# Optimization experiments

Measured on AMD Instinct MI355X. Metric: run time of the kernel, lower is better.

## Reference

```python
import jax, jax.numpy as jnp
import numpy as np
import math

B, S, H = 2, 2048, 2048
NH, NKV, HD = 16, 8, 128          # heads, kv heads, head_dim
GROUPS = NH // NKV                 # 2
FF = 5632
EPS = 1e-6
SCALE = 0.02


def setup_inputs() -> dict:
    key = jax.random.key(0)
    ks = jax.random.split(key, 12)
    def w(k, shape):
        return jax.random.normal(k, shape, dtype=jnp.float32) * SCALE
    # additive causal mask: 0 on/below diagonal, -inf above
    causal = jnp.where(jnp.tril(jnp.ones((S, S), dtype=bool)), 0.0, -jnp.inf)
    attention_mask = causal[None, None].astype(jnp.float32)  # [1,1,S,S]
    return {
        "hidden_states": jax.random.normal(ks[0], (B, S, H), dtype=jnp.float32),
        "attention_mask": attention_mask,
        "q_w": w(ks[1], (NH * HD, H)),      # nn.Linear convention [out, in]
        "k_w": w(ks[2], (NKV * HD, H)),
        "v_w": w(ks[3], (NKV * HD, H)),
        "o_w": w(ks[4], (H, NH * HD)),
        "gate_w": w(ks[5], (FF, H)),
        "up_w": w(ks[6], (FF, H)),
        "down_w": w(ks[7], (H, FF)),
        "ln1_w": jnp.ones((H,), dtype=jnp.float32),
        "ln2_w": jnp.ones((H,), dtype=jnp.float32),
    }


def rmsnorm(x, w):
    var = jnp.mean(jnp.square(x), axis=-1, keepdims=True)
    return x * jax.lax.rsqrt(var + EPS) * w


def attention(x, mask, q_w, k_w, v_w, o_w):
    b, s, _ = x.shape
    q = (x @ q_w.T).reshape(b, s, NH, HD).transpose(0, 2, 1, 3)    # [b,nh,s,hd]
    k = (x @ k_w.T).reshape(b, s, NKV, HD).transpose(0, 2, 1, 3)   # [b,nkv,s,hd]
    v = (x @ v_w.T).reshape(b, s, NKV, HD).transpose(0, 2, 1, 3)
    # GQA: repeat_interleave kv heads to match query heads
    k = jnp.repeat(k, GROUPS, axis=1)
    v = jnp.repeat(v, GROUPS, axis=1)
    scores = jnp.einsum("bhqd,bhkd->bhqk", q, k) / math.sqrt(HD) + mask
    probs = jax.nn.softmax(scores.astype(jnp.float32), axis=-1).astype(q.dtype)
    out = jnp.einsum("bhqk,bhkd->bhqd", probs, v)
    out = out.transpose(0, 2, 1, 3).reshape(b, s, NH * HD)
    return out @ o_w.T


def mlp(x, gate_w, up_w, down_w):
    return (jax.nn.silu(x @ gate_w.T) * (x @ up_w.T)) @ down_w.T


def reference(hidden_states, attention_mask, q_w, k_w, v_w, o_w,
              gate_w, up_w, down_w, ln1_w, ln2_w):
    # pre-norm transformer layer with residuals
    h = hidden_states + attention(rmsnorm(hidden_states, ln1_w), attention_mask,
                                  q_w, k_w, v_w, o_w)
    out = h + mlp(rmsnorm(h, ln2_w), gate_w, up_w, down_w)
    return out
```

## Files before the change

kernel.cpp:

```cpp
#include <hip/hip_runtime.h>
#include <stdint.h>

typedef __bf16 bf16_t;
typedef __bf16 bf16x8 __attribute__((ext_vector_type(8)));
typedef __bf16 bf16x4 __attribute__((ext_vector_type(4)));
typedef float  f32x4  __attribute__((ext_vector_type(4)));

#define MFMA16(a, b, c) __builtin_amdgcn_mfma_f32_16x16x32_bf16((a), (b), (c), 0, 0, 0)

__device__ __forceinline__ void load_lds16(const bf16_t* g, bf16_t* l)
{
    __builtin_amdgcn_global_load_lds(
        (const __attribute__((address_space(1))) uint32_t*)(uintptr_t)g,
        (__attribute__((address_space(3))) uint32_t*)(uint32_t)(uintptr_t)l,
        16, 0, 0);
}

__device__ __forceinline__ void lds_stage2(const bf16_t* __restrict__ Gsrc,
                                           bf16_t* Ldst, int u0,
                                           int tid, int K, int k0)
{
#pragma unroll
    for (int l = 0; l < 2; ++l) {
        int u = u0 + l * 512 + tid;
// ... 49 lines not shown
}

__global__ __launch_bounds__(256)
void rmsnorm_bf16(const bf16_t* __restrict__ X, const float* __restrict__ Wt,
                  bf16_t* __restrict__ Y)
{
    __shared__ float red[4];
    const int tid = threadIdx.x;
    const size_t row = blockIdx.x;

    bf16x8 xv = *(const bf16x8*)(X + row * 2048 + tid * 8);
    float xf[8];
    float ss = 0.f;
#pragma unroll
    for (int e = 0; e < 8; ++e) { xf[e] = (float)xv[e]; ss += xf[e] * xf[e]; }
#pragma unroll
    for (int off = 32; off; off >>= 1) ss += __shfl_xor(ss, off, 64);
    if ((tid & 63) == 0) red[tid >> 6] = ss;
    __syncthreads();
    float tot = red[0] + red[1] + red[2] + red[3];
    float scale = rsqrtf(tot * (1.f / 2048.f) + 1e-6f);

    f32x4 w0 = *(const f32x4*)(Wt + tid * 8);
    f32x4 w1 = *(const f32x4*)(Wt + tid * 8 + 4);
    bf16x8 yv;
#pragma unroll
    for (int e = 0; e < 4; ++e) {
        yv[e]     = (bf16_t)(xf[e] * scale * w0[e]);
        yv[e + 4] = (bf16_t)(xf[e + 4] * scale * w1[e]);
    }
    *(bf16x8*)(Y + row * 2048 + tid * 8) = yv;
}

__global__ __launch_bounds__(256, 2)
void gemm_bb(const bf16_t* __restrict__ A, const bf16_t* __restrict__ W,
             const float* __restrict__ Rf, const bf16_t* __restrict__ Rb,
             bf16_t* __restrict__ Cb, float* __restrict__ Cf,
             int M, int N, int K, int mode)
{
    __shared__ bf16_t As[128 * 64];
    __shared__ bf16_t Ws[128 * 64];

    const int tid  = threadIdx.x;
    const int lane = tid & 63, wave = tid >> 6;
    const int quad = lane >> 4, l16 = lane & 15;
    const int m0 = blockIdx.y * 128, n0 = blockIdx.x * 128;
    const int wm = (wave >> 1) * 64, wn = (wave & 1) * 64;

    const bf16_t* Ab = A + (size_t)(m0 + (tid >> 3)) * K + ((tid & 7) << 3);
    const bf16_t* Wb = W + (size_t)(n0 + (tid >> 3)) * K + ((tid & 7) << 3);

    f32x4 acc[4][4] = {};

    for (int k0 = 0; k0 < K; k0 += 64) {
        __syncthreads();
#pragma unroll
        for (int i = 0; i < 4; ++i) {
            load_lds16(Ab + (size_t)(i * 32) * K + k0, As + (i * 256 + tid) * 8);
            load_lds16(Wb + (size_t)(i * 32) * K + k0, Ws + (i * 256 + tid) * 8);
        }
        __syncthreads();

#pragma unroll
        for (int ks = 0; ks < 64; ks += 32) {
            bf16x8 af[4], bfr[4];
#pragma unroll
            for (int i = 0; i < 4; ++i)
                af[i] = *(const bf16x8*)(As + (wm + i * 16 + l16) * 64 + ks + quad * 8);
#pragma unroll
            for (int j = 0; j < 4; ++j)
                bfr[j] = *(const bf16x8*)(Ws + (wn + j * 16 + l16) * 64 + ks + quad * 8);
#pragma unroll
            for (int i = 0; i < 4; ++i)
#pragma unroll
                for (int j = 0; j < 4; ++j)
                    acc[i][j] = MFMA16(af[i], bfr[j], acc[i][j]);
        }
    }

#pragma unroll
    for (int i = 0; i < 4; ++i)
#pragma unroll
        for (int j = 0; j < 4; ++j)
#pragma unroll
            for (int r = 0; r < 4; ++r) {
                size_t row = (size_t)(m0 + wm + i * 16 + quad * 4 + r);
                size_t col = (size_t)(n0 + wn + j * 16 + l16);
                float v = acc[i][j][r];
                if (mode == 1) v += Rf[row * (size_t)N + col];
                if (mode == 2)
                    Cf[row * (size_t)N + col] = v + (float)Rb[row * (size_t)N + col];
                else
                    Cb[row * (size_t)N + col] = (bf16_t)v;
            }
}

__global__ __launch_bounds__(512, 2)
void gemm8(const bf16_t* __restrict__ A, const bf16_t* __restrict__ W,
           const float* __restrict__ Rf, const bf16_t* __restrict__ Rb,
           bf16_t* __restrict__ Cb, float* __restrict__ Cf,
           int M, int N, int K, int mode)
{
    __shared__ bf16_t As[2][256 * 64];
    __shared__ bf16_t Ws[2][128 * 64];

    const int tid  = threadIdx.x;
    const int lane = tid & 63, wave = tid >> 6;
    const int quad = lane >> 4, l16 = lane & 15;
    const int wr = wave >> 1, wc = wave & 1;

    const int lid = (int)blockIdx.x;
    const int swz = (lid & 7) * 32 + (lid >> 3);
    const int bym = swz >> 4;
    const int bxn = swz & 15;
    const int m0 = bym * 256, n0 = bxn * 128;

    const bf16_t* Ab = A + (size_t)m0 * K;
    const bf16_t* Wb = W + (size_t)n0 * K;

    const int xsw  = (l16 & 7) << 3;
    const int aoff = (wr * 64 + l16) * 64;
    const int boff = (wc * 64 + l16) * 64;

    f32x4 acc[4][4] = {};

    lds_stage2(Ab, As[0], 0,    tid, K, 0);
    lds_stage2(Ab, As[0], 1024, tid, K, 0);
    lds_stage2(Wb, Ws[0], 0,    tid, K, 0);

    const int NT = K >> 6;
    for (int t = 0; t < NT; ++t) {
        const int b  = t & 1;
        const int kn = (t + 1) << 6;
        const bool pf = (t + 1 < NT);
        bf16_t* An = As[1 - b];
        bf16_t* Wn = Ws[1 - b];

        if (pf) {
            lds_stage2(Ab, An, 0, tid, K, kn);
            asm volatile("s_waitcnt vmcnt(2)" ::: "memory");
        } else {
            asm volatile("s_waitcnt vmcnt(0)" ::: "memory");
        }
        __builtin_amdgcn_s_barrier();

        const bf16_t* Asb = As[b];
        const bf16_t* Wsb = Ws[b];

#pragma unroll
        for (int ks = 0; ks < 2; ++ks) {
            const int kxo = (ks * 32 + quad * 8) ^ xsw;
            bf16x8 af[4], bf_[4];
#pragma unroll
            for (int i = 0; i < 4; ++i)
                af[i] = *(const bf16x8*)(Asb + aoff + i * 1024 + kxo);
#pragma unroll
            for (int j = 0; j < 4; ++j)
                bf_[j] = *(const bf16x8*)(Wsb + boff + j * 1024 + kxo);
            if (pf) {
                if (ks == 0) lds_stage2(Ab, An, 1024, tid, K, kn);
                else         lds_stage2(Wb, Wn, 0,    tid, K, kn);
            }
            __builtin_amdgcn_s_barrier();
            __builtin_amdgcn_s_setprio(1);
#pragma unroll
            for (int i = 0; i < 4; ++i)
#pragma unroll
                for (int j = 0; j < 4; ++j)
                    acc[i][j] = MFMA16(af[i], bf_[j], acc[i][j]);
            __builtin_amdgcn_s_setprio(0);
            __builtin_amdgcn_s_barrier();
        }
    }

#pragma unroll
    for (int i = 0; i < 4; ++i)
#pragma unroll
        for (int j = 0; j < 4; ++j)
#pragma unroll
            for (int r = 0; r < 4; ++r) {
                size_t row = (size_t)(m0 + wr * 64 + i * 16 + quad * 4 + r);
                size_t col = (size_t)(n0 + wc * 64 + j * 16 + l16);
                float v = acc[i][j][r];
                if (mode == 1) v += Rf[row * (size_t)N + col];
                if (mode == 2)
                    Cf[row * (size_t)N + col] = v + (float)Rb[row * (size_t)N + col];
                else
                    Cb[row * (size_t)N + col] = (bf16_t)v;
            }
}

__global__ __launch_bounds__(512, 2)
void gateup8(const bf16_t* __restrict__ A, const bf16_t* __restrict__ G,
             const bf16_t* __restrict__ U, bf16_t* __restrict__ C,
             int M, int N, int K)
{
    __shared__ bf16_t As[2][256 * 64];
    __shared__ bf16_t Gs[2][128 * 64];
    __shared__ bf16_t Us[2][128 * 64];

    const int tid  = threadIdx.x;
    const int lane = tid & 63;
    const int wave = tid >> 6;
    const int quad = lane >> 4, l16 = lane & 15;
    const int wr = wave >> 2, wc = wave & 3;

    const int lid = (int)blockIdx.x;
    const int nwg = (M >> 8) * (N >> 7);
    const int cpx = nwg >> 3;
    const int swz = (lid & 7) * cpx + (lid >> 3);
    const int bxn = swz >> 4;
    const int bym = swz & 15;
    const int m0 = bym * 256, n0 = bxn * 128;

    const bf16_t* Ab = A + (size_t)m0 * K;
    const bf16_t* Gb = G + (size_t)n0 * K;
    const bf16_t* Ub = U + (size_t)n0 * K;

    const int xsw  = (l16 & 7) << 3;
    const int aoff = (wr * 128 + l16) * 64;
    const int boff = (wc * 32 + l16) * 64;

    f32x4 accg[8][2] = {};
    f32x4 accu[8][2] = {};

    lds_stage2(Ab, As[0], 0,    tid, K, 0);
    lds_stage2(Ab, As[0], 1024, tid, K, 0);
    lds_stage2(Gb, Gs[0], 0,    tid, K, 0);
    lds_stage2(Ub, Us[0], 0,    tid, K, 0);

    const int NT = K >> 6;
    for (int t = 0; t < NT; ++t) {
        const int b  = t & 1;
        const int kn = (t + 1) << 6;
        const bool pf = (t + 1 < NT);
        bf16_t* An = As[1 - b];
        bf16_t* Gn = Gs[1 - b];
        bf16_t* Un = Us[1 - b];

        if (pf) {
            lds_stage2(Ab, An, 0, tid, K, kn);
            asm volatile("s_waitcnt vmcnt(2)" ::: "memory");
        } else {
            asm volatile("s_waitcnt vmcnt(0)" ::: "memory");
        }
        __builtin_amdgcn_s_barrier();

        const bf16_t* Asb = As[b];
        const bf16_t* Gsb = Gs[b];
        const bf16_t* Usb = Us[b];

        bf16x8 af[4], bg[2], bu[2];

        {
            const int kxo = (quad * 8) ^ xsw;
#pragma unroll
            for (int i = 0; i < 4; ++i)
                af[i] = *(const bf16x8*)(Asb + aoff + i * 1024 + kxo);
#pragma unroll
            for (int j = 0; j < 2; ++j) {
                bg[j] = *(const bf16x8*)(Gsb + boff + j * 1024 + kxo);
                bu[j] = *(const bf16x8*)(Usb + boff + j * 1024 + kxo);
            }
        }
        if (pf) lds_stage2(Ab, An, 1024, tid, K, kn);
        __builtin_amdgcn_s_barrier();
        __builtin_amdgcn_s_setprio(1);
#pragma unroll
        for (int i = 0; i < 4; ++i)
#pragma unroll
            for (int j = 0; j < 2; ++j) {
                accg[i][j] = MFMA16(af[i], bg[j], accg[i][j]);
                accu[i][j] = MFMA16(af[i], bu[j], accu[i][j]);
            }
        __builtin_amdgcn_s_setprio(0);
        __builtin_amdgcn_s_barrier();

        {
            const int kxo = (quad * 8) ^ xsw;
#pragma unroll
            for (int i = 0; i < 4; ++i)
                af[i] = *(const bf16x8*)(Asb + aoff + (i + 4) * 1024 + kxo);
        }
        if (pf) lds_stage2(Gb, Gn, 0, tid, K, kn);
        __builtin_amdgcn_s_barrier();
        __builtin_amdgcn_s_setprio(1);
#pragma unroll
        for (int i = 0; i < 4; ++i)
#pragma unroll
            for (int j = 0; j < 2; ++j) {
                accg[i + 4][j] = MFMA16(af[i], bg[j], accg[i + 4][j]);
                accu[i + 4][j] = MFMA16(af[i], bu[j], accu[i + 4][j]);
            }
        __builtin_amdgcn_s_setprio(0);
        __builtin_amdgcn_s_barrier();

        {
            const int kxo = (32 + quad * 8) ^ xsw;
#pragma unroll
            for (int i = 0; i < 4; ++i)
                af[i] = *(const bf16x8*)(Asb + aoff + i * 1024 + kxo);
#pragma unroll
            for (int j = 0; j < 2; ++j) {
                bg[j] = *(const bf16x8*)(Gsb + boff + j * 1024 + kxo);
                bu[j] = *(const bf16x8*)(Usb + boff + j * 1024 + kxo);
            }
        }
        if (pf) lds_stage2(Ub, Un, 0, tid, K, kn);
        __builtin_amdgcn_s_barrier();
        __builtin_amdgcn_s_setprio(1);
#pragma unroll
        for (int i = 0; i < 4; ++i)
#pragma unroll
            for (int j = 0; j < 2; ++j) {
                accg[i][j] = MFMA16(af[i], bg[j], accg[i][j]);
                accu[i][j] = MFMA16(af[i], bu[j], accu[i][j]);
            }
        __builtin_amdgcn_s_setprio(0);
        __builtin_amdgcn_s_barrier();

        {
            const int kxo = (32 + quad * 8) ^ xsw;
#pragma unroll
            for (int i = 0; i < 4; ++i)
                af[i] = *(const bf16x8*)(Asb + aoff + (i + 4) * 1024 + kxo);
        }
        __builtin_amdgcn_s_barrier();
        __builtin_amdgcn_s_setprio(1);
#pragma unroll
        for (int i = 0; i < 4; ++i)
#pragma unroll
            for (int j = 0; j < 2; ++j) {
                accg[i + 4][j] = MFMA16(af[i], bg[j], accg[i + 4][j]);
                accu[i + 4][j] = MFMA16(af[i], bu[j], accu[i + 4][j]);
            }
        __builtin_amdgcn_s_setprio(0);
        __builtin_amdgcn_s_barrier();
    }

#pragma unroll
    for (int i = 0; i < 8; ++i)
#pragma unroll
        for (int j = 0; j < 2; ++j)
#pragma unroll
            for (int r = 0; r < 4; ++r) {
                size_t row = (size_t)(m0 + wr * 128 + i * 16 + quad * 4 + r);
                size_t col = (size_t)(n0 + wc * 32 + j * 16 + l16);
                float g = accg[i][j][r];
                float u = accu[i][j][r];
                float sig = 1.f / (1.f + __expf(fminf(-g, 80.f)));
                C[row * (size_t)N + col] = (bf16_t)(g * sig * u);
            }
}

__global__ __launch_bounds__(256, 2)
void gemm_bt(const bf16_t* __restrict__ A, const float* __restrict__ W,
             const float* __restrict__ Rf, const bf16_t* __restrict__ Rb,
             bf16_t* __restrict__ Cb, float* __restrict__ Cf,
             int M, int N, int K, int mode)
{
    __shared__ bf16_t As[128 * 64];
    __shared__ bf16_t Ws[128 * 64];

    const int tid  = threadIdx.x;
    const int lane = tid & 63, wave = tid >> 6;
    const int quad = lane >> 4, l16 = lane & 15;
    const int m0 = blockIdx.y * 128, n0 = blockIdx.x * 128;
    const int wm = (wave >> 1) * 64, wn = (wave & 1) * 64;

    f32x4 acc[4][4] = {};

    for (int k0 = 0; k0 < K; k0 += 64) {
        bf16x8 ra[4];
        bf16x4 rw[8];
#pragma unroll
        for (int i = 0; i < 4; ++i) {
            int u = i * 256 + tid;
            int r = u >> 3, c = (u & 7) << 3;
            ra[i] = *(const bf16x8*)(A + (size_t)(m0 + r) * K + k0 + c);
        }
#pragma unroll
        for (int i = 0; i < 8; ++i) {
            int u = i * 256 + tid;
            int r = u >> 4, c = (u & 15) << 2;
            f32x4 w4 = *(const f32x4*)(W + (size_t)(n0 + r) * K + k0 + c);
#pragma unroll
            for (int e = 0; e < 4; ++e) rw[i][e] = (bf16_t)w4[e];
        }
        __syncthreads();
#pragma unroll
        for (int i = 0; i < 4; ++i)
            *(bf16x8*)(As + (i * 256 + tid) * 8) = ra[i];
#pragma unroll
        for (int i = 0; i < 8; ++i)
            *(bf16x4*)(Ws + (i * 256 + tid) * 4) = rw[i];
        __syncthreads();

#pragma unroll
        for (int ks = 0; ks < 64; ks += 32) {
            bf16x8 af[4], bfr[4];
#pragma unroll
            for (int i = 0; i < 4; ++i)
                af[i] = *(const bf16x8*)(As + (wm + i * 16 + l16) * 64 + ks + quad * 8);
#pragma unroll
            for (int j = 0; j < 4; ++j)
                bfr[j] = *(const bf16x8*)(Ws + (wn + j * 16 + l16) * 64 + ks + quad * 8);
#pragma unroll
            for (int i = 0; i < 4; ++i)
#pragma unroll
                for (int j = 0; j < 4; ++j)
                    acc[i][j] = MFMA16(af[i], bfr[j], acc[i][j]);
        }
    }

#pragma unroll
    for (int i = 0; i < 4; ++i)
#pragma unroll
        for (int j = 0; j < 4; ++j)
#pragma unroll
            for (int r = 0; r < 4; ++r) {
                size_t row = (size_t)(m0 + wm + i * 16 + quad * 4 + r);
                size_t col = (size_t)(n0 + wn + j * 16 + l16);
                float v = acc[i][j][r];
                if (mode == 1) v += Rf[row * (size_t)N + col];
                if (mode == 2)
                    Cf[row * (size_t)N + col] = v + (float)Rb[row * (size_t)N + col];
                else
                    Cb[row * (size_t)N + col] = (bf16_t)v;
            }
}

__global__ __launch_bounds__(256, 2)
void gemm_gateup(const bf16_t* __restrict__ A, const float* __restrict__ G,
                 const float* __restrict__ U, bf16_t* __restrict__ C,
                 int M, int N, int K)
{
    __shared__ bf16_t As[128 * 64];
    __shared__ bf16_t Gs[128 * 64];
    __shared__ bf16_t Us[128 * 64];

    const int tid  = threadIdx.x;
    const int lane = tid & 63, wave = tid >> 6;
    const int quad = lane >> 4, l16 = lane & 15;
    const int m0 = blockIdx.y * 128, n0 = blockIdx.x * 128;
    const int wm = (wave >> 1) * 64, wn = (wave & 1) * 64;

    f32x4 accg[4][4] = {};
    f32x4 accu[4][4] = {};

    for (int k0 = 0; k0 < K; k0 += 64) {
        bf16x8 ra[4];
        bf16x4 rg[8], ru[8];
#pragma unroll
        for (int i = 0; i < 4; ++i) {
            int u = i * 256 + tid;
            int r = u >> 3, c = (u & 7) << 3;
            ra[i] = *(const bf16x8*)(A + (size_t)(m0 + r) * K + k0 + c);
        }
#pragma unroll
        for (int i = 0; i < 8; ++i) {
            int u = i * 256 + tid;
            int r = u >> 4, c = (u & 15) << 2;
            f32x4 g4 = *(const f32x4*)(G + (size_t)(n0 + r) * K + k0 + c);
            f32x4 u4 = *(const f32x4*)(U + (size_t)(n0 + r) * K + k0 + c);
// ... 19 lines not shown
                af[i] = *(const bf16x8*)(As + (wm + i * 16 + l16) * 64 + ks + quad * 8);
#pragma unroll
            for (int j = 0; j < 4; ++j) {
                bg[j] = *(const bf16x8*)(Gs + (wn + j * 16 + l16) * 64 + ks + quad * 8);
                bu[j] = *(const bf16x8*)(Us + (wn + j * 16 + l16) * 64 + ks + quad * 8);
            }
#pragma unroll
            for (int i = 0; i < 4; ++i)
#pragma unroll
                for (int j = 0; j < 4; ++j) {
                    accg[i][j] = MFMA16(af[i], bg[j], accg[i][j]);
                    accu[i][j] = MFMA16(af[i], bu[j], accu[i][j]);
                }
        }
    }

#pragma unroll
    for (int i = 0; i < 4; ++i)
#pragma unroll
        for (int j = 0; j < 4; ++j)
#pragma unroll
            for (int r = 0; r < 4; ++r) {
                size_t row = (size_t)(m0 + wm + i * 16 + quad * 4 + r);
                size_t col = (size_t)(n0 + wn + j * 16 + l16);
                float g = accg[i][j][r];
                float u = accu[i][j][r];
                float sig = 1.f / (1.f + __expf(fminf(-g, 80.f)));
                C[row * (size_t)N + col] = (bf16_t)(g * sig * u);
            }
}

__global__ __launch_bounds__(256, 2)
void attn_fwd(const bf16_t* __restrict__ Q, const bf16_t* __restrict__ Kg,
              const bf16_t* __restrict__ Vg, bf16_t* __restrict__ O)
{
    __shared__ bf16_t Ks[64 * 128];
    __shared__ bf16_t Vt[128 * 64];
    __shared__ bf16_t Pl[4][16 * 72];

    const int tid  = threadIdx.x;
    const int lane = tid & 63, wave = tid >> 6;
    const int quad = lane >> 4, l16 = lane & 15;
    const int bh = blockIdx.y, b = bh >> 4, h = bh & 15;

    const bf16_t* Qh = Q  + (size_t)b * 2048 * 2048 + (size_t)h * 128;
    const bf16_t* Kh = Kg + (size_t)b * 2048 * 1024 + (size_t)(h >> 1) * 128;
    const bf16_t* Vh = Vg + (size_t)b * 2048 * 1024 + (size_t)(h >> 1) * 128;

    const float scale = 0.08838834764831845f;

#pragma unroll 1
    for (int pass = 0; pass < 2; ++pass) {
        const int qt = pass ? (31 - (int)blockIdx.x) : (int)blockIdx.x;
        const int q0 = qt * 64;

        bf16x8 aq[4];
#pragma unroll
        for (int ks = 0; ks < 4; ++ks)
            aq[ks] = *(const bf16x8*)(Qh + (size_t)(q0 + wave * 16 + l16) * 2048 + ks * 32 + quad * 8);

        float m_r[4] = { -30000.f, -30000.f, -30000.f, -30000.f };
        float l_r[4] = { 0.f, 0.f, 0.f, 0.f };
        f32x4 acc_o[8] = {};

        const int ntiles = qt + 1;

        for (int t = 0; t < ntiles; ++t) {
            const int kv0 = t * 64;
            __syncthreads();
#pragma unroll
            for (int i = 0; i < 4; ++i) {
                int u = i * 256 + tid;
                int rk = u >> 4, c = (u & 15) << 3;
                *(bf16x8*)(Ks + u * 8) =
                    *(const bf16x8*)(Kh + (size_t)(kv0 + rk) * 1024 + c);
            }
#pragma unroll
            for (int it = 0; it < 4; ++it) {
                int v = it * 256 + tid;
                int d = v & 127, kb = v >> 7;
                bf16x8 vt8;
#pragma unroll
                for (int j = 0; j < 8; ++j)
                    vt8[j] = Vh[(size_t)(kv0 + kb * 8 + j) * 1024 + d];
                *(bf16x8*)(Vt + d * 64 + ((kb ^ (d & 7)) << 3)) = vt8;
            }
            __syncthreads();

            f32x4 accs[4] = {};
#pragma unroll
            for (int ks = 0; ks < 4; ++ks)
#pragma unroll
                for (int j = 0; j < 4; ++j) {
                    bf16x8 bk = *(const bf16x8*)(Ks + (j * 16 + l16) * 128 + ks * 32 + quad * 8);
                    accs[j] = MFMA16(aq[ks], bk, accs[j]);
                }

#pragma unroll
            for (int r = 0; r < 4; ++r) {
                const int qrow = q0 + wave * 16 + quad * 4 + r;
                float s[4];
                float mx = -30000.f;
#pragma unroll
                for (int j = 0; j < 4; ++j) {
                    s[j] = accs[j][r] * scale;
                    if (kv0 + j * 16 + l16 > qrow) s[j] = -30000.f;
                    mx = fmaxf(mx, s[j]);
                }
                mx = fmaxf(mx, __shfl_xor(mx, 1, 64));
                mx = fmaxf(mx, __shfl_xor(mx, 2, 64));
                mx = fmaxf(mx, __shfl_xor(mx, 4, 64));
                mx = fmaxf(mx, __shfl_xor(mx, 8, 64));
                float mnew  = fmaxf(m_r[r], mx);
                float alpha = __expf(fmaxf(m_r[r] - mnew, -80.f));
                float rs = 0.f;
#pragma unroll
                for (int j = 0; j < 4; ++j) {
                    float p = __expf(fmaxf(s[j] - mnew, -80.f));
                    rs += p;
                    Pl[wave][(quad * 4 + r) * 72 + j * 16 + l16] = (bf16_t)p;
                }
                rs += __shfl_xor(rs, 1, 64);
                rs += __shfl_xor(rs, 2, 64);
                rs += __shfl_xor(rs, 4, 64);
                rs += __shfl_xor(rs, 8, 64);
                l_r[r] = l_r[r] * alpha + rs;
                m_r[r] = mnew;
#pragma unroll
                for (int nt = 0; nt < 8; ++nt) acc_o[nt][r] *= alpha;
            }

            __syncthreads();

#pragma unroll
            for (int ks2 = 0; ks2 < 2; ++ks2) {
                bf16x8 ap = *(const bf16x8*)(&Pl[wave][l16 * 72 + ks2 * 32 + quad * 8]);
                const int kb_r = ks2 * 4 + quad;
#pragma unroll
                for (int nt = 0; nt < 8; ++nt) {
                    const int d = nt * 16 + l16;
                    bf16x8 bv = *(const bf16x8*)(Vt + d * 64 + ((kb_r ^ (d & 7)) << 3));
                    acc_o[nt] = MFMA16(ap, bv, acc_o[nt]);
                }
            }
        }

#pragma unroll
        for (int r = 0; r < 4; ++r) {
            float inv = 1.f / fmaxf(l_r[r], 1e-30f);
            size_t orow = (size_t)b * 2048 + q0 + wave * 16 + quad * 4 + r;
#pragma unroll
            for (int nt = 0; nt < 8; ++nt)
                O[orow * 2048 + h * 128 + nt * 16 + l16] = (bf16_t)(acc_o[nt][r] * inv);
        }
    }
}

extern "C" void kernel_launch(void* const* d_in, const int* in_sizes, int n_in,
                              void* d_out, int out_size, void* d_ws, size_t ws_size,
                              hipStream_t stream)
{
    const float* x   = (const float*)d_in[0];
    const float* qw  = (const float*)d_in[2];
    const float* kw  = (const float*)d_in[3];
    const float* vw  = (const float*)d_in[4];
    const float* ow  = (const float*)d_in[5];
    const float* gw  = (const float*)d_in[6];
    const float* uw  = (const float*)d_in[7];
    const float* dw  = (const float*)d_in[8];
    const float* ln1 = (const float*)d_in[9];
    const float* ln2 = (const float*)d_in[10];
    float*  out = (float*)d_out;
    bf16_t* ws  = (bf16_t*)d_ws;

    dim3 blk(256);
    const size_t NEED = 87031808ull * 2;

    if (ws_size >= NEED) {
        bf16_t* wq = ws;
        bf16_t* wk = ws + 4194304;
        bf16_t* wv = ws + 6291456;
        bf16_t* wo = ws + 8388608;
        bf16_t* wg = ws + 12582912;
        bf16_t* wu = ws + 24117248;
        bf16_t* wd = ws + 35651584;
        bf16_t* h1 = ws + 47185920;
        bf16_t* qb = ws + 55574528;
        bf16_t* kb = ws + 63963136;
        bf16_t* vb = ws + 68157440;
        bf16_t* ab = (bf16_t*)d_out;
        bf16_t* hb = qb;
        bf16_t* gb = kb;

        wconv<<<2048, blk, 0, stream>>>(qw, wq, 4194304);
        wconv<<<1024, blk, 0, stream>>>(kw, wk, 2097152);
        wconv<<<1024, blk, 0, stream>>>(vw, wv, 2097152);
        wconv<<<2048, blk, 0, stream>>>(ow, wo, 4194304);
        wconv<<<5632, blk, 0, stream>>>(gw, wg, 11534336);
        wconv<<<5632, blk, 0, stream>>>(uw, wu, 11534336);
        wconv<<<5632, blk, 0, stream>>>(dw, wd, 11534336);

        rmsnorm_f32<<<4096, blk, 0, stream>>>(x, ln1, h1);
        gemm8<<<256, dim3(512), 0, stream>>>(h1, wq, nullptr, nullptr, qb, nullptr, 4096, 2048, 2048, 0);
        gemm_bb<<<dim3( 8, 32), blk, 0, stream>>>(h1, wk, nullptr, nullptr, kb, nullptr, 4096, 1024, 2048, 0);
        gemm_bb<<<dim3( 8, 32), blk, 0, stream>>>(h1, wv, nullptr, nullptr, vb, nullptr, 4096, 1024, 2048, 0);
        attn_fwd<<<dim3(16, 32), blk, 0, stream>>>(qb, kb, vb, ab);
        gemm8<<<256, dim3(512), 0, stream>>>(ab, wo, x, nullptr, hb, nullptr, 4096, 2048, 2048, 1);
        rmsnorm_bf16<<<4096, blk, 0, stream>>>(hb, ln2, h1);
        gateup8<<<704, dim3(512), 0, stream>>>(h1, wg, wu, gb, 4096, 5632, 2048);
        gemm8<<<256, dim3(512), 0, stream>>>(gb, wd, nullptr, hb, nullptr, out, 4096, 2048, 5632, 2);
    } else {
        const size_t ME = 1ull << 20;
        bf16_t* h1 = ws;
        bf16_t* qb = ws + 8  * ME;
        bf16_t* kb = ws + 16 * ME;
        bf16_t* vb = ws + 20 * ME;
        bf16_t* ab = (bf16_t*)d_out;
        bf16_t* hb = ws + 8  * ME;
        bf16_t* gb = ws + 16 * ME;

        rmsnorm_f32<<<4096, blk, 0, stream>>>(x, ln1, h1);
        gemm_bt<<<dim3(16, 32), blk, 0, stream>>>(h1, qw, nullptr, nullptr, qb, nullptr, 4096, 2048, 2048, 0);
        gemm_bt<<<dim3( 8, 32), blk, 0, stream>>>(h1, kw, nullptr, nullptr, kb, nullptr, 4096, 1024, 2048, 0);
        gemm_bt<<<dim3( 8, 32), blk, 0, stream>>>(h1, vw, nullptr, nullptr, vb, nullptr, 4096, 1024, 2048, 0);
        attn_fwd<<<dim3(16, 32), blk, 0, stream>>>(qb, kb, vb, ab);
        gemm_bt<<<dim3(16, 32), blk, 0, stream>>>(ab, ow, x, nullptr, hb, nullptr, 4096, 2048, 2048, 1);
        rmsnorm_bf16<<<4096, blk, 0, stream>>>(hb, ln2, h1);
        gemm_gateup<<<dim3(44, 32), blk, 0, stream>>>(h1, gw, uw, gb, 4096, 5632, 2048);
        gemm_bt<<<dim3(16, 32), blk, 0, stream>>>(gb, dw, nullptr, hb, nullptr, out, 4096, 2048, 5632, 2);
    }
}
```

Measured before the change: 887.2 us.

## Fuse K/V projections into one gemm8 launch and double-buffer attention KV tiles

The separate K and V projection GEMMs (the older 128x128 gemm_bb kernel) become a single launch of the pipelined 256x128 gemm8 kernel. A new epilogue mode splits the output columns between the K and V buffers, which relies on wk and wv sitting next to each other in the workspace. The attention kernel now double-buffers its K and V^T LDS tiles with a register prefetch of the next tile, K is stored with an XOR swizzle, and one barrier per iteration is removed. gemm8's block swizzle is also generalised through an nbx parameter. The risks are higher LDS use in attention, which may lower occupancy, and a dependence on the weight layout.

```diff
diff --git a/kernel.cpp b/kernel.cpp
--- a/kernel.cpp
+++ b/kernel.cpp
@@ -105,8 +105,273 @@
     *(bf16x8*)(Y + row * 2048 + tid * 8) = yv;
 }
 
+__global__ __launch_bounds__(512, 2)
+void gemm8(const bf16_t* __restrict__ A, const bf16_t* __restrict__ W,
+           const float* __restrict__ Rf, const bf16_t* __restrict__ Rb,
+           bf16_t* __restrict__ Cb, bf16_t* __restrict__ Cb2,
+           float* __restrict__ Cf,
+           int M, int N, int K, int nbx, int mode)
+{
+    __shared__ bf16_t As[2][256 * 64];
+    __shared__ bf16_t Ws[2][128 * 64];
+
+    const int tid  = threadIdx.x;
+    const int lane = tid & 63, wave = tid >> 6;
+    const int quad = lane >> 4, l16 = lane & 15;
+    const int wr = wave >> 1, wc = wave & 1;
+
+    const int lid = (int)blockIdx.x;
+    const int nwg = (M >> 8) * nbx;
+    const int q   = nwg >> 3;
+    const int swz = (lid & 7) * q + (lid >> 3);
+    const int bxn = swz >> 4;
+    const int bym = swz & 15;
+    const int m0 = bym * 256, n0 = bxn * 128;
+
+    const bf16_t* Ab = A + (size_t)m0 * K;
+    const bf16_t* Wb = W + (size_t)n0 * K;
+
+    const int xsw  = (l16 & 7) << 3;
+    const int aoff = (wr * 64 + l16) * 64;
+    const int boff = (wc * 64 + l16) * 64;
+
+    f32x4 acc[4][4] = {};
+
+    lds_stage2(Ab, As[0], 0,    tid, K, 0);
+    lds_stage2(Ab, As[0], 1024, tid, K, 0);
+    lds_stage2(Wb, Ws[0], 0,    tid, K, 0);
+
+    const int NT = K >> 6;
+    for (int t = 0; t < NT; ++t) {
+        const int b  = t & 1;
+        const int kn = (t + 1) << 6;
+        const bool pf = (t + 1 < NT);
+        bf16_t* An = As[1 - b];
+        bf16_t* Wn = Ws[1 - b];
+
+        if (pf) {
+            lds_stage2(Ab, An, 0, tid, K, kn);
+            asm volatile("s_waitcnt vmcnt(2)" ::: "memory");
+        } else {
+            asm volatile("s_waitcnt vmcnt(0)" ::: "memory");
+        }
+        __builtin_amdgcn_s_barrier();
+
+        const bf16_t* Asb = As[b];
+        const bf16_t* Wsb = Ws[b];
+
+#pragma unroll
+        for (int ks = 0; ks < 2; ++ks) {
+            const int kxo = (ks * 32 + quad * 8) ^ xsw;
+            bf16x8 af[4], bf_[4];
+#pragma unroll
+            for (int i = 0; i < 4; ++i)
+                af[i] = *(const bf16x8*)(Asb + aoff + i * 1024 + kxo);
+#pragma unroll
+            for (int j = 0; j < 4; ++j)
+                bf_[j] = *(const bf16x8*)(Wsb + boff + j * 1024 + kxo);
+            if (pf) {
+                if (ks == 0) lds_stage2(Ab, An, 1024, tid, K, kn);
+                else         lds_stage2(Wb, Wn, 0,    tid, K, kn);
+            }
+            __builtin_amdgcn_s_barrier();
+            __builtin_amdgcn_s_setprio(1);
+#pragma unroll
+            for (int i = 0; i < 4; ++i)
+#pragma unroll
+                for (int j = 0; j < 4; ++j)
+                    acc[i][j] = MFMA16(af[i], bf_[j], acc[i][j]);
+            __builtin_amdgcn_s_setprio(0);
+            __builtin_amdgcn_s_barrier();
+        }
+    }
+
+    bf16_t* dst5 = (n0 < 1024) ? Cb : Cb2;
+
+#pragma unroll
+    for (int i = 0; i < 4; ++i)
+#pragma unroll
+        for (int j = 0; j < 4; ++j)
+#pragma unroll
+            for (int r = 0; r < 4; ++r) {
+                size_t row = (size_t)(m0 + wr * 64 + i * 16 + quad * 4 + r);
+                size_t col = (size_t)(n0 + wc * 64 + j * 16 + l16);
+                float v = acc[i][j][r];
+                if (mode == 1) v += Rf[row * (size_t)N + col];
+                if (mode == 2)
+                    Cf[row * (size_t)N + col] = v + (float)Rb[row * (size_t)N + col];
+                else if (mode == 5)
+                    dst5[row * 1024 + (col & 1023)] = (bf16_t)v;
+                else
+                    Cb[row * (size_t)N + col] = (bf16_t)v;
+            }
+}
+
+__global__ __launch_bounds__(512, 2)
+void gateup8(const bf16_t* __restrict__ A, const bf16_t* __restrict__ G,
+             const bf16_t* __restrict__ U, bf16_t* __restrict__ C,
+             int M, int N, int K)
+{
+    __shared__ bf16_t As[2][256 * 64];
+    __shared__ bf16_t Gs[2][128 * 64];
+    __shared__ bf16_t Us[2][128 * 64];
+
+    const int tid  = threadIdx.x;
+    const int lane = tid & 63;
+    const int wave = tid >> 6;
+    const int quad = lane >> 4, l16 = lane & 15;
+    const int wr = wave >> 2, wc = wave & 3;
+
+    const int lid = (int)blockIdx.x;
+    const int nwg = (M >> 8) * (N >> 7);
+    const int cpx = nwg >> 3;
+    const int swz = (lid & 7) * cpx + (lid >> 3);
+    const int bxn = swz >> 4;
+    const int bym = swz & 15;
+    const int m0 = bym * 256, n0 = bxn * 128;
+
+    const bf16_t* Ab = A + (size_t)m0 * K;
+    const bf16_t* Gb = G + (size_t)n0 * K;
+    const bf16_t* Ub = U + (size_t)n0 * K;
+
+    const int xsw  = (l16 & 7) << 3;
+    const int aoff = (wr * 128 + l16) * 64;
+    const int boff = (wc * 32 + l16) * 64;
+
+    f32x4 accg[8][2] = {};
+    f32x4 accu[8][2] = {};
+
+    lds_stage2(Ab, As[0], 0,    tid, K, 0);
+    lds_stage2(Ab, As[0], 1024, tid, K, 0);
+    lds_stage2(Gb, Gs[0], 0,    tid, K, 0);
+    lds_stage2(Ub, Us[0], 0,    tid, K, 0);
+
+    const int NT = K >> 6;
+    for (int t = 0; t < NT; ++t) {
+        const int b  = t & 1;
+        const int kn = (t + 1) << 6;
+        const bool pf = (t + 1 < NT);
+        bf16_t* An = As[1 - b];
+        bf16_t* Gn = Gs[1 - b];
+        bf16_t* Un = Us[1 - b];
+
+        if (pf) {
+            lds_stage2(Ab, An, 0, tid, K, kn);
+            asm volatile("s_waitcnt vmcnt(2)" ::: "memory");
+        } else {
+            asm volatile("s_waitcnt vmcnt(0)" ::: "memory");
+        }
+        __builtin_amdgcn_s_barrier();
+
+        const bf16_t* Asb = As[b];
+        const bf16_t* Gsb = Gs[b];
+        const bf16_t* Usb = Us[b];
+
+        bf16x8 af[4], bg[2], bu[2];
+
+        {
+            const int kxo = (quad * 8) ^ xsw;
+#pragma unroll
+            for (int i = 0; i < 4; ++i)
+                af[i] = *(const bf16x8*)(Asb + aoff + i * 1024 + kxo);
+#pragma unroll
+            for (int j = 0; j < 2; ++j) {
+                bg[j] = *(const bf16x8*)(Gsb + boff + j * 1024 + kxo);
+                bu[j] = *(const bf16x8*)(Usb + boff + j * 1024 + kxo);
+            }
+        }
+        if (pf) lds_stage2(Ab, An, 1024, tid, K, kn);
+        __builtin_amdgcn_s_barrier();
+        __builtin_amdgcn_s_setprio(1);
+#pragma unroll
+        for (int i = 0; i < 4; ++i)
+#pragma unroll
+            for (int j = 0; j < 2; ++j) {
+                accg[i][j] = MFMA16(af[i], bg[j], accg[i][j]);
+                accu[i][j] = MFMA16(af[i], bu[j], accu[i][j]);
+            }
+        __builtin_amdgcn_s_setprio(0);
+        __builtin_amdgcn_s_barrier();
+
+        {
+            const int kxo = (quad * 8) ^ xsw;
+#pragma unroll
+            for (int i = 0; i < 4; ++i)
+                af[i] = *(const bf16x8*)(Asb + aoff + (i + 4) * 1024 + kxo);
+        }
+        if (pf) lds_stage2(Gb, Gn, 0, tid, K, kn);
+        __builtin_amdgcn_s_barrier();
+        __builtin_amdgcn_s_setprio(1);
+#pragma unroll
+        for (int i = 0; i < 4; ++i)
+#pragma unroll
+            for (int j = 0; j < 2; ++j) {
+                accg[i + 4][j] = MFMA16(af[i], bg[j], accg[i + 4][j]);
+                accu[i + 4][j] = MFMA16(af[i], bu[j], accu[i + 4][j]);
+            }
+        __builtin_amdgcn_s_setprio(0);
+        __builtin_amdgcn_s_barrier();
+
+        {
+            const int kxo = (32 + quad * 8) ^ xsw;
+#pragma unroll
+            for (int i = 0; i < 4; ++i)
+                af[i] = *(const bf16x8*)(Asb + aoff + i * 1024 + kxo);
+#pragma unroll
+            for (int j = 0; j < 2; ++j) {
+                bg[j] = *(const bf16x8*)(Gsb + boff + j * 1024 + kxo);
+                bu[j] = *(const bf16x8*)(Usb + boff + j * 1024 + kxo);
+            }
+        }
+        if (pf) lds_stage2(Ub, Un, 0, tid, K, kn);
+        __builtin_amdgcn_s_barrier();
+        __builtin_amdgcn_s_setprio(1);
+#pragma unroll
+        for (int i = 0; i < 4; ++i)
+#pragma unroll
+            for (int j = 0; j < 2; ++j) {
+                accg[i][j] = MFMA16(af[i], bg[j], accg[i][j]);
+                accu[i][j] = MFMA16(af[i], bu[j], accu[i][j]);
+            }
+        __builtin_amdgcn_s_setprio(0);
+        __builtin_amdgcn_s_barrier();
+
+        {
+            const int kxo = (32 + quad * 8) ^ xsw;
+#pragma unroll
+            for (int i = 0; i < 4; ++i)
+                af[i] = *(const bf16x8*)(Asb + aoff + (i + 4) * 1024 + kxo);
+        }
+        __builtin_amdgcn_s_barrier();
+        __builtin_amdgcn_s_setprio(1);
+#pragma unroll
+        for (int i = 0; i < 4; ++i)
+#pragma unroll
+            for (int j = 0; j < 2; ++j) {
+                accg[i + 4][j] = MFMA16(af[i], bg[j], accg[i + 4][j]);
+                accu[i + 4][j] = MFMA16(af[i], bu[j], accu[i + 4][j]);
+            }
+        __builtin_amdgcn_s_setprio(0);
+        __builtin_amdgcn_s_barrier();
+    }
+
+#pragma unroll
+    for (int i = 0; i < 8; ++i)
+#pragma unroll
+        for (int j = 0; j < 2; ++j)
+#pragma unroll
+            for (int r = 0; r < 4; ++r) {
+                size_t row = (size_t)(m0 + wr * 128 + i * 16 + quad * 4 + r);
+                size_t col = (size_t)(n0 + wc * 32 + j * 16 + l16);
+                float g = accg[i][j][r];
+                float u = accu[i][j][r];
+                float sig = 1.f / (1.f + __expf(fminf(-g, 80.f)));
+                C[row * (size_t)N + col] = (bf16_t)(g * sig * u);
+            }
+}
+
 __global__ __launch_bounds__(256, 2)
-void gemm_bb(const bf16_t* __restrict__ A, const bf16_t* __restrict__ W,
+void gemm_bt(const bf16_t* __restrict__ A, const float* __restrict__ W,
              const float* __restrict__ Rf, const bf16_t* __restrict__ Rb,
              bf16_t* __restrict__ Cb, float* __restrict__ Cf,
              int M, int N, int K, int mode)
@@ -120,18 +385,32 @@
     const int m0 = blockIdx.y * 128, n0 = blockIdx.x * 128;
     const int wm = (wave >> 1) * 64, wn = (wave & 1) * 64;
 
-    const bf16_t* Ab = A + (size_t)(m0 + (tid >> 3)) * K + ((tid & 7) << 3);
-    const bf16_t* Wb = W + (size_t)(n0 + (tid >> 3)) * K + ((tid & 7) << 3);
-
     f32x4 acc[4][4] = {};
 
     for (int k0 = 0; k0 < K; k0 += 64) {
+        bf16x8 ra[4];
+        bf16x4 rw[8];
+#pragma unroll
+        for (int i = 0; i < 4; ++i) {
+            int u = i * 256 + tid;
+            int r = u >> 3, c = (u & 7) << 3;
+            ra[i] = *(const bf16x8*)(A + (size_t)(m0 + r) * K + k0 + c);
+        }
+#pragma unroll
+        for (int i = 0; i < 8; ++i) {
+            int u = i * 256 + tid;
+            int r = u >> 4, c = (u & 15) << 2;
+            f32x4 w4 = *(const f32x4*)(W + (size_t)(n0 + r) * K + k0 + c);
+#pragma unroll
+            for (int e = 0; e < 4; ++e) rw[i][e] = (bf16_t)w4[e];
+        }
         __syncthreads();
 #pragma unroll
-        for (int i = 0; i < 4; ++i) {
-            load_lds16(Ab + (size_t)(i * 32) * K + k0, As + (i * 256 + tid) * 8);
-            load_lds16(Wb + (size_t)(i * 32) * K + k0, Ws + (i * 256 + tid) * 8);
-        }
+        for (int i = 0; i < 4; ++i)
+            *(bf16x8*)(As + (i * 256 + tid) * 8) = ra[i];
+#pragma unroll
+        for (int i = 0; i < 8; ++i)
+            *(bf16x4*)(Ws + (i * 256 + tid) * 4) = rw[i];
         __syncthreads();
 
 #pragma unroll
@@ -168,341 +447,6 @@
             }
 }
 
-__global__ __launch_bounds__(512, 2)
-void gemm8(const bf16_t* __restrict__ A, const bf16_t* __restrict__ W,
-           const float* __restrict__ Rf, const bf16_t* __restrict__ Rb,
-           bf16_t* __restrict__ Cb, float* __restrict__ Cf,
-           int M, int N, int K, int mode)
-{
-    __shared__ bf16_t As[2][256 * 64];
-    __shared__ bf16_t Ws[2][128 * 64];
-
-    const int tid  = threadIdx.x;
-    const int lane = tid & 63, wave = tid >> 6;
-    const int quad = lane >> 4, l16 = lane & 15;
-    const int wr = wave >> 1, wc = wave & 1;
-
-    const int lid = (int)blockIdx.x;
-    const int swz = (lid & 7) * 32 + (lid >> 3);
-    const int bym = swz >> 4;
-    const int bxn = swz & 15;
-    const int m0 = bym * 256, n0 = bxn * 128;
-
-    const bf16_t* Ab = A + (size_t)m0 * K;
-    const bf16_t* Wb = W + (size_t)n0 * K;
-
-    const int xsw  = (l16 & 7) << 3;
-    const int aoff = (wr * 64 + l16) * 64;
-    const int boff = (wc * 64 + l16) * 64;
-
-    f32x4 acc[4][4] = {};
-
-    lds_stage2(Ab, As[0], 0,    tid, K, 0);
-    lds_stage2(Ab, As[0], 1024, tid, K, 0);
-    lds_stage2(Wb, Ws[0], 0,    tid, K, 0);
-
-    const int NT = K >> 6;
-    for (int t = 0; t < NT; ++t) {
-        const int b  = t & 1;
-        const int kn = (t + 1) << 6;
-        const bool pf = (t + 1 < NT);
-        bf16_t* An = As[1 - b];
-        bf16_t* Wn = Ws[1 - b];
-
-        if (pf) {
-            lds_stage2(Ab, An, 0, tid, K, kn);
-            asm volatile("s_waitcnt vmcnt(2)" ::: "memory");
-        } else {
-            asm volatile("s_waitcnt vmcnt(0)" ::: "memory");
-        }
-        __builtin_amdgcn_s_barrier();
-
-        const bf16_t* Asb = As[b];
-        const bf16_t* Wsb = Ws[b];
-
-#pragma unroll
-        for (int ks = 0; ks < 2; ++ks) {
-            const int kxo = (ks * 32 + quad * 8) ^ xsw;
-            bf16x8 af[4], bf_[4];
-#pragma unroll
-            for (int i = 0; i < 4; ++i)
-                af[i] = *(const bf16x8*)(Asb + aoff + i * 1024 + kxo);
-#pragma unroll
-            for (int j = 0; j < 4; ++j)
-                bf_[j] = *(const bf16x8*)(Wsb + boff + j * 1024 + kxo);
-            if (pf) {
-                if (ks == 0) lds_stage2(Ab, An, 1024, tid, K, kn);
-                else         lds_stage2(Wb, Wn, 0,    tid, K, kn);
-            }
-            __builtin_amdgcn_s_barrier();
-            __builtin_amdgcn_s_setprio(1);
-#pragma unroll
-            for (int i = 0; i < 4; ++i)
-#pragma unroll
-                for (int j = 0; j < 4; ++j)
-                    acc[i][j] = MFMA16(af[i], bf_[j], acc[i][j]);
-            __builtin_amdgcn_s_setprio(0);
-            __builtin_amdgcn_s_barrier();
-        }
-    }
-
-#pragma unroll
-    for (int i = 0; i < 4; ++i)
-#pragma unroll
-        for (int j = 0; j < 4; ++j)
-#pragma unroll
-            for (int r = 0; r < 4; ++r) {
-                size_t row = (size_t)(m0 + wr * 64 + i * 16 + quad * 4 + r);
-                size_t col = (size_t)(n0 + wc * 64 + j * 16 + l16);
-                float v = acc[i][j][r];
-                if (mode == 1) v += Rf[row * (size_t)N + col];
-                if (mode == 2)
-                    Cf[row * (size_t)N + col] = v + (float)Rb[row * (size_t)N + col];
-                else
-                    Cb[row * (size_t)N + col] = (bf16_t)v;
-            }
-}
-
-__global__ __launch_bounds__(512, 2)
-void gateup8(const bf16_t* __restrict__ A, const bf16_t* __restrict__ G,
-             const bf16_t* __restrict__ U, bf16_t* __restrict__ C,
-             int M, int N, int K)
-{
-    __shared__ bf16_t As[2][256 * 64];
-    __shared__ bf16_t Gs[2][128 * 64];
-    __shared__ bf16_t Us[2][128 * 64];
-
-    const int tid  = threadIdx.x;
-    const int lane = tid & 63;
-    const int wave = tid >> 6;
-    const int quad = lane >> 4, l16 = lane & 15;
-    const int wr = wave >> 2, wc = wave & 3;
-
-    const int lid = (int)blockIdx.x;
-    const int nwg = (M >> 8) * (N >> 7);
-    const int cpx = nwg >> 3;
-    const int swz = (lid & 7) * cpx + (lid >> 3);
-    const int bxn = swz >> 4;
-    const int bym = swz & 15;
-    const int m0 = bym * 256, n0 = bxn * 128;
-
-    const bf16_t* Ab = A + (size_t)m0 * K;
-    const bf16_t* Gb = G + (size_t)n0 * K;
-    const bf16_t* Ub = U + (size_t)n0 * K;
-
-    const int xsw  = (l16 & 7) << 3;
-    const int aoff = (wr * 128 + l16) * 64;
-    const int boff = (wc * 32 + l16) * 64;
-
-    f32x4 accg[8][2] = {};
-    f32x4 accu[8][2] = {};
-
-    lds_stage2(Ab, As[0], 0,    tid, K, 0);
-    lds_stage2(Ab, As[0], 1024, tid, K, 0);
-    lds_stage2(Gb, Gs[0], 0,    tid, K, 0);
-    lds_stage2(Ub, Us[0], 0,    tid, K, 0);
-
-    const int NT = K >> 6;
-    for (int t = 0; t < NT; ++t) {
-        const int b  = t & 1;
-        const int kn = (t + 1) << 6;
-        const bool pf = (t + 1 < NT);
-        bf16_t* An = As[1 - b];
-        bf16_t* Gn = Gs[1 - b];
-        bf16_t* Un = Us[1 - b];
-
-        if (pf) {
-            lds_stage2(Ab, An, 0, tid, K, kn);
-            asm volatile("s_waitcnt vmcnt(2)" ::: "memory");
-        } else {
-            asm volatile("s_waitcnt vmcnt(0)" ::: "memory");
-        }
-        __builtin_amdgcn_s_barrier();
-
-        const bf16_t* Asb = As[b];
-        const bf16_t* Gsb = Gs[b];
-        const bf16_t* Usb = Us[b];
-
-        bf16x8 af[4], bg[2], bu[2];
-
-        {
-            const int kxo = (quad * 8) ^ xsw;
-#pragma unroll
-            for (int i = 0; i < 4; ++i)
-                af[i] = *(const bf16x8*)(Asb + aoff + i * 1024 + kxo);
-#pragma unroll
-            for (int j = 0; j < 2; ++j) {
-                bg[j] = *(const bf16x8*)(Gsb + boff + j * 1024 + kxo);
-                bu[j] = *(const bf16x8*)(Usb + boff + j * 1024 + kxo);
-            }
-        }
-        if (pf) lds_stage2(Ab, An, 1024, tid, K, kn);
-        __builtin_amdgcn_s_barrier();
-        __builtin_amdgcn_s_setprio(1);
-#pragma unroll
-        for (int i = 0; i < 4; ++i)
-#pragma unroll
-            for (int j = 0; j < 2; ++j) {
-                accg[i][j] = MFMA16(af[i], bg[j], accg[i][j]);
-                accu[i][j] = MFMA16(af[i], bu[j], accu[i][j]);
-            }
-        __builtin_amdgcn_s_setprio(0);
-        __builtin_amdgcn_s_barrier();
-
-        {
-            const int kxo = (quad * 8) ^ xsw;
-#pragma unroll
-            for (int i = 0; i < 4; ++i)
-                af[i] = *(const bf16x8*)(Asb + aoff + (i + 4) * 1024 + kxo);
-        }
-        if (pf) lds_stage2(Gb, Gn, 0, tid, K, kn);
-        __builtin_amdgcn_s_barrier();
-        __builtin_amdgcn_s_setprio(1);
-#pragma unroll
-        for (int i = 0; i < 4; ++i)
-#pragma unroll
-            for (int j = 0; j < 2; ++j) {
-                accg[i + 4][j] = MFMA16(af[i], bg[j], accg[i + 4][j]);
-                accu[i + 4][j] = MFMA16(af[i], bu[j], accu[i + 4][j]);
-            }
-        __builtin_amdgcn_s_setprio(0);
-        __builtin_amdgcn_s_barrier();
-
-        {
-            const int kxo = (32 + quad * 8) ^ xsw;
-#pragma unroll
-            for (int i = 0; i < 4; ++i)
-                af[i] = *(const bf16x8*)(Asb + aoff + i * 1024 + kxo);
-#pragma unroll
-            for (int j = 0; j < 2; ++j) {
-                bg[j] = *(const bf16x8*)(Gsb + boff + j * 1024 + kxo);
-                bu[j] = *(const bf16x8*)(Usb + boff + j * 1024 + kxo);
-            }
-        }
-        if (pf) lds_stage2(Ub, Un, 0, tid, K, kn);
-        __builtin_amdgcn_s_barrier();
-        __builtin_amdgcn_s_setprio(1);
-#pragma unroll
-        for (int i = 0; i < 4; ++i)
-#pragma unroll
-            for (int j = 0; j < 2; ++j) {
-                accg[i][j] = MFMA16(af[i], bg[j], accg[i][j]);
-                accu[i][j] = MFMA16(af[i], bu[j], accu[i][j]);
-            }
-        __builtin_amdgcn_s_setprio(0);
-        __builtin_amdgcn_s_barrier();
-
-        {
-            const int kxo = (32 + quad * 8) ^ xsw;
-#pragma unroll
-            for (int i = 0; i < 4; ++i)
-                af[i] = *(const bf16x8*)(Asb + aoff + (i + 4) * 1024 + kxo);
-        }
-        __builtin_amdgcn_s_barrier();
-        __builtin_amdgcn_s_setprio(1);
-#pragma unroll
-        for (int i = 0; i < 4; ++i)
-#pragma unroll
-            for (int j = 0; j < 2; ++j) {
-                accg[i + 4][j] = MFMA16(af[i], bg[j], accg[i + 4][j]);
-                accu[i + 4][j] = MFMA16(af[i], bu[j], accu[i + 4][j]);
-            }
-        __builtin_amdgcn_s_setprio(0);
-        __builtin_amdgcn_s_barrier();
-    }
-
-#pragma unroll
-    for (int i = 0; i < 8; ++i)
-#pragma unroll
-        for (int j = 0; j < 2; ++j)
-#pragma unroll
-            for (int r = 0; r < 4; ++r) {
-                size_t row = (size_t)(m0 + wr * 128 + i * 16 + quad * 4 + r);
-                size_t col = (size_t)(n0 + wc * 32 + j * 16 + l16);
-                float g = accg[i][j][r];
-                float u = accu[i][j][r];
-                float sig = 1.f / (1.f + __expf(fminf(-g, 80.f)));
-                C[row * (size_t)N + col] = (bf16_t)(g * sig * u);
-            }
-}
-
-__global__ __launch_bounds__(256, 2)
-void gemm_bt(const bf16_t* __restrict__ A, const float* __restrict__ W,
-             const float* __restrict__ Rf, const bf16_t* __restrict__ Rb,
-             bf16_t* __restrict__ Cb, float* __restrict__ Cf,
-             int M, int N, int K, int mode)
-{
-    __shared__ bf16_t As[128 * 64];
-    __shared__ bf16_t Ws[128 * 64];
-
-    const int tid  = threadIdx.x;
-    const int lane = tid & 63, wave = tid >> 6;
-    const int quad = lane >> 4, l16 = lane & 15;
-    const int m0 = blockIdx.y * 128, n0 = blockIdx.x * 128;
-    const int wm = (wave >> 1) * 64, wn = (wave & 1) * 64;
-
-    f32x4 acc[4][4] = {};
-
-    for (int k0 = 0; k0 < K; k0 += 64) {
-        bf16x8 ra[4];
-        bf16x4 rw[8];
-#pragma unroll
-        for (int i = 0; i < 4; ++i) {
-            int u = i * 256 + tid;
-            int r = u >> 3, c = (u & 7) << 3;
-            ra[i] = *(const bf16x8*)(A + (size_t)(m0 + r) * K + k0 + c);
-        }
-#pragma unroll
-        for (int i = 0; i < 8; ++i) {
-            int u = i * 256 + tid;
-            int r = u >> 4, c = (u & 15) << 2;
-            f32x4 w4 = *(const f32x4*)(W + (size_t)(n0 + r) * K + k0 + c);
-#pragma unroll
-            for (int e = 0; e < 4; ++e) rw[i][e] = (bf16_t)w4[e];
-        }
-        __syncthreads();
-#pragma unroll
-        for (int i = 0; i < 4; ++i)
-            *(bf16x8*)(As + (i * 256 + tid) * 8) = ra[i];
-#pragma unroll
-        for (int i = 0; i < 8; ++i)
-            *(bf16x4*)(Ws + (i * 256 + tid) * 4) = rw[i];
-        __syncthreads();
-
-#pragma unroll
-        for (int ks = 0; ks < 64; ks += 32) {
-            bf16x8 af[4], bfr[4];
-#pragma unroll
-            for (int i = 0; i < 4; ++i)
-                af[i] = *(const bf16x8*)(As + (wm + i * 16 + l16) * 64 + ks + quad * 8);
-#pragma unroll
-            for (int j = 0; j < 4; ++j)
-                bfr[j] = *(const bf16x8*)(Ws + (wn + j * 16 + l16) * 64 + ks + quad * 8);
-#pragma unroll
-            for (int i = 0; i < 4; ++i)
-#pragma unroll
-                for (int j = 0; j < 4; ++j)
-                    acc[i][j] = MFMA16(af[i], bfr[j], acc[i][j]);
-        }
-    }
-
-#pragma unroll
-    for (int i = 0; i < 4; ++i)
-#pragma unroll
-        for (int j = 0; j < 4; ++j)
-#pragma unroll
-            for (int r = 0; r < 4; ++r) {
-                size_t row = (size_t)(m0 + wm + i * 16 + quad * 4 + r);
-                size_t col = (size_t)(n0 + wn + j * 16 + l16);
-                float v = acc[i][j][r];
-                if (mode == 1) v += Rf[row * (size_t)N + col];
-                if (mode == 2)
-                    Cf[row * (size_t)N + col] = v + (float)Rb[row * (size_t)N + col];
-                else
-                    Cb[row * (size_t)N + col] = (bf16_t)v;
-            }
-}
-
 __global__ __launch_bounds__(256, 2)
 void gemm_gateup(const bf16_t* __restrict__ A, const float* __restrict__ G,
                  const float* __restrict__ U, bf16_t* __restrict__ C,
@@ -588,10 +532,10 @@
 
 __global__ __launch_bounds__(256, 2)
 void attn_fwd(const bf16_t* __restrict__ Q, const bf16_t* __restrict__ Kg,
-              const bf16_t* __restrict__ Vg, bf16_t* __restrict__ O)
-{
-    __shared__ bf16_t Ks[64 * 128];
-    __shared__ bf16_t Vt[128 * 64];
+              const bf16_t* __restrict__ Vg, bf16_t* __restrict__ O, int kvs)
+{
+    __shared__ bf16_t Ks[2][64 * 128];
+    __shared__ bf16_t Vt[2][128 * 64];
     __shared__ bf16_t Pl[4][16 * 72];
 
     const int tid  = threadIdx.x;
@@ -600,10 +544,15 @@
     const int bh = blockIdx.y, b = bh >> 4, h = bh & 15;
 
     const bf16_t* Qh = Q  + (size_t)b * 2048 * 2048 + (size_t)h * 128;
-    const bf16_t* Kh = Kg + (size_t)b * 2048 * 1024 + (size_t)(h >> 1) * 128;
-    const bf16_t* Vh = Vg + (size_t)b * 2048 * 1024 + (size_t)(h >> 1) * 128;
+    const bf16_t* Kh = Kg + (size_t)b * 2048 * kvs + (size_t)(h >> 1) * 128;
+    const bf16_t* Vh = Vg + (size_t)b * 2048 * kvs + (size_t)(h >> 1) * 128;
 
     const float scale = 0.08838834764831845f;
+
+    const int krow = tid >> 4;
+    const int kcol = (tid & 15) << 3;
+    const int vd   = tid & 127;
+    const int vkb  = tid >> 7;
 
 #pragma unroll 1
     for (int pass = 0; pass < 2; ++pass) {
@@ -621,34 +570,51 @@
 
         const int ntiles = qt + 1;
 
+        bf16x8 rk[4], rv[4];
+#pragma unroll
+        for (int i = 0; i < 4; ++i)
+            rk[i] = *(const bf16x8*)(Kh + (size_t)(i * 16 + krow) * kvs + kcol);
+#pragma unroll
+        for (int it = 0; it < 4; ++it)
+#pragma unroll
+            for (int j = 0; j < 8; ++j)
+                rv[it][j] = Vh[(size_t)((vkb + 2 * it) * 8 + j) * kvs + vd];
+#pragma unroll
+        for (int i = 0; i < 4; ++i) {
+            int row = i * 16 + krow;
+            *(bf16x8*)(&Ks[0][row * 128 + (kcol ^ ((row & 7) << 3))]) = rk[i];
+        }
+#pragma unroll
+        for (int it = 0; it < 4; ++it) {
+            int kb = vkb + 2 * it;
+            *(bf16x8*)(&Vt[0][vd * 64 + ((kb ^ (vd & 7)) << 3)]) = rv[it];
+        }
+        __syncthreads();
+
         for (int t = 0; t < ntiles; ++t) {
+            const int bb = t & 1;
+            const bool pf = (t + 1 < ntiles);
             const int kv0 = t * 64;
-            __syncthreads();
-#pragma unroll
-            for (int i = 0; i < 4; ++i) {
-                int u = i * 256 + tid;
-                int rk = u >> 4, c = (u & 15) << 3;
-                *(bf16x8*)(Ks + u * 8) =
-                    *(const bf16x8*)(Kh + (size_t)(kv0 + rk) * 1024 + c);
-            }
-#pragma unroll
-            for (int it = 0; it < 4; ++it) {
-                int v = it * 256 + tid;
-                int d = v & 127, kb = v >> 7;
-                bf16x8 vt8;
-#pragma unroll
-                for (int j = 0; j < 8; ++j)
-                    vt8[j] = Vh[(size_t)(kv0 + kb * 8 + j) * 1024 + d];
-                *(bf16x8*)(Vt + d * 64 + ((kb ^ (d & 7)) << 3)) = vt8;
-            }
-            __syncthreads();
+            const int kvn = kv0 + 64;
+
+            if (pf) {
+#pragma unroll
+                for (int i = 0; i < 4; ++i)
+                    rk[i] = *(const bf16x8*)(Kh + (size_t)(kvn + i * 16 + krow) * kvs + kcol);
+#pragma unroll
+                for (int it = 0; it < 4; ++it)
+#pragma unroll
+                    for (int j = 0; j < 8; ++j)
+                        rv[it][j] = Vh[(size_t)(kvn + (vkb + 2 * it) * 8 + j) * kvs + vd];
+            }
 
             f32x4 accs[4] = {};
 #pragma unroll
             for (int ks = 0; ks < 4; ++ks)
 #pragma unroll
                 for (int j = 0; j < 4; ++j) {
-                    bf16x8 bk = *(const bf16x8*)(Ks + (j * 16 + l16) * 128 + ks * 32 + quad * 8);
+                    const int row = j * 16 + l16;
+                    bf16x8 bk = *(const bf16x8*)(&Ks[bb][row * 128 + ((ks * 32 + quad * 8) ^ ((row & 7) << 3))]);
                     accs[j] = MFMA16(aq[ks], bk, accs[j]);
                 }
 
@@ -686,8 +652,6 @@
                 for (int nt = 0; nt < 8; ++nt) acc_o[nt][r] *= alpha;
             }
 
-            __syncthreads();
-
 #pragma unroll
             for (int ks2 = 0; ks2 < 2; ++ks2) {
                 bf16x8 ap = *(const bf16x8*)(&Pl[wave][l16 * 72 + ks2 * 32 + quad * 8]);
@@ -695,10 +659,24 @@
 #pragma unroll
                 for (int nt = 0; nt < 8; ++nt) {
                     const int d = nt * 16 + l16;
-                    bf16x8 bv = *(const bf16x8*)(Vt + d * 64 + ((kb_r ^ (d & 7)) << 3));
+                    bf16x8 bv = *(const bf16x8*)(&Vt[bb][d * 64 + ((kb_r ^ (d & 7)) << 3)]);
                     acc_o[nt] = MFMA16(ap, bv, acc_o[nt]);
                 }
             }
+
+            if (pf) {
+#pragma unroll
+                for (int i = 0; i < 4; ++i) {
+                    int row = i * 16 + krow;
+                    *(bf16x8*)(&Ks[1 - bb][row * 128 + (kcol ^ ((row & 7) << 3))]) = rk[i];
+                }
+#pragma unroll
+                for (int it = 0; it < 4; ++it) {
+                    int kb = vkb + 2 * it;
+                    *(bf16x8*)(&Vt[1 - bb][vd * 64 + ((kb ^ (vd & 7)) << 3)]) = rv[it];
+                }
+            }
+            __syncthreads();
         }
 
 #pragma unroll
@@ -757,14 +735,13 @@
         wconv<<<5632, blk, 0, stream>>>(dw, wd, 11534336);
 
         rmsnorm_f32<<<4096, blk, 0, stream>>>(x, ln1, h1);
-        gemm8<<<256, dim3(512), 0, stream>>>(h1, wq, nullptr, nullptr, qb, nullptr, 4096, 2048, 2048, 0);
-        gemm_bb<<<dim3( 8, 32), blk, 0, stream>>>(h1, wk, nullptr, nullptr, kb, nullptr, 4096, 1024, 2048, 0);
-        gemm_bb<<<dim3( 8, 32), blk, 0, stream>>>(h1, wv, nullptr, nullptr, vb, nullptr, 4096, 1024, 2048, 0);
-        attn_fwd<<<dim3(16, 32), blk, 0, stream>>>(qb, kb, vb, ab);
-        gemm8<<<256, dim3(512), 0, stream>>>(ab, wo, x, nullptr, hb, nullptr, 4096, 2048, 2048, 1);
+        gemm8<<<256, dim3(512), 0, stream>>>(h1, wq, nullptr, nullptr, qb, nullptr, nullptr, 4096, 2048, 2048, 16, 0);
+        gemm8<<<256, dim3(512), 0, stream>>>(h1, wk, nullptr, nullptr, kb, vb, nullptr, 4096, 2048, 2048, 16, 5);
+        attn_fwd<<<dim3(16, 32), blk, 0, stream>>>(qb, kb, vb, ab, 1024);
+        gemm8<<<256, dim3(512), 0, stream>>>(ab, wo, x, nullptr, hb, nullptr, nullptr, 4096, 2048, 2048, 16, 1);
         rmsnorm_bf16<<<4096, blk, 0, stream>>>(hb, ln2, h1);
         gateup8<<<704, dim3(512), 0, stream>>>(h1, wg, wu, gb, 4096, 5632, 2048);
-        gemm8<<<256, dim3(512), 0, stream>>>(gb, wd, nullptr, hb, nullptr, out, 4096, 2048, 5632, 2);
+        gemm8<<<256, dim3(512), 0, stream>>>(gb, wd, nullptr, hb, nullptr, nullptr, out, 4096, 2048, 5632, 16, 2);
     } else {
         const size_t ME = 1ull << 20;
         bf16_t* h1 = ws;
@@ -779,7 +756,7 @@
         gemm_bt<<<dim3(16, 32), blk, 0, stream>>>(h1, qw, nullptr, nullptr, qb, nullptr, 4096, 2048, 2048, 0);
         gemm_bt<<<dim3( 8, 32), blk, 0, stream>>>(h1, kw, nullptr, nullptr, kb, nullptr, 4096, 1024, 2048, 0);
         gemm_bt<<<dim3( 8, 32), blk, 0, stream>>>(h1, vw, nullptr, nullptr, vb, nullptr, 4096, 1024, 2048, 0);
-        attn_fwd<<<dim3(16, 32), blk, 0, stream>>>(qb, kb, vb, ab);
+        attn_fwd<<<dim3(16, 32), blk, 0, stream>>>(qb, kb, vb, ab, 1024);
         gemm_bt<<<dim3(16, 32), blk, 0, stream>>>(ab, ow, x, nullptr, hb, nullptr, 4096, 2048, 2048, 1);
         rmsnorm_bf16<<<4096, blk, 0, stream>>>(hb, ln2, h1);
         gemm_gateup<<<dim3(44, 32), blk, 0, stream>>>(h1, gw, uw, gb, 4096, 5632, 2048);
```

Result: faster. 818.8 us (-7.7%).
